# Performance work log

Measured on AMD Instinct MI355X. Metric: run time of the kernel, lower is better.

## Reference

```python
import jax, jax.numpy as jnp
import numpy as np

N_NODES = 50000


def _gcn_conv(x, src, dst, norm, W, b):
    # x: [N, F_in], src/dst: [E+N] (self loops included), norm: [E+N]
    h = x @ W                                   # [N, F_out]
    msg = h[src] * norm[:, None]                # [E+N, F_out] gather + scale
    out = jax.ops.segment_sum(msg, dst, num_segments=N_NODES)  # scatter-add
    return out + b


def _norm_coeffs(edge_index, n_nodes):
    # PyG GCNConv: add self loops, deg over dst (col), norm = d^-1/2[src]*d^-1/2[dst]
    loops = jnp.arange(n_nodes, dtype=edge_index.dtype)
    src = jnp.concatenate([edge_index[0], loops])
    dst = jnp.concatenate([edge_index[1], loops])
    deg = jax.ops.segment_sum(jnp.ones_like(dst, dtype=jnp.float32), dst,
                              num_segments=n_nodes)
    dinv = jnp.where(deg > 0, jax.lax.rsqrt(jnp.maximum(deg, 1.0)), 0.0)
    norm = dinv[src] * dinv[dst]
    return src, dst, norm


def setup_inputs() -> dict:
    key = jax.random.key(0)
    ks = jax.random.split(key, 8)
    F_in, F_hid, E = 128, 128, 600000
    x = jax.random.normal(ks[0], (N_NODES, F_in), dtype=jnp.float32)
    edge_index = jax.random.randint(ks[1], (2, E), 0, N_NODES, dtype=jnp.int32)
    s1 = 1.0 / np.sqrt(F_in)
    s2 = 1.0 / np.sqrt(F_hid)
    W1 = jax.random.uniform(ks[2], (F_in, F_hid), jnp.float32, -s1, s1)
    b1 = jnp.zeros((F_hid,), jnp.float32)
    W2 = jax.random.uniform(ks[3], (F_hid, F_hid), jnp.float32, -s2, s2)
    b2 = jnp.zeros((F_hid,), jnp.float32)
    W3 = jax.random.uniform(ks[4], (F_hid, F_hid), jnp.float32, -s2, s2)
    b3 = jnp.zeros((F_hid,), jnp.float32)
    return {"x": x, "edge_index": edge_index,
            "W1": W1, "b1": b1, "W2": W2, "b2": b2, "W3": W3, "b3": b3}


def reference(x, edge_index, W1, b1, W2, b2, W3, b3):
    src, dst, norm = _norm_coeffs(edge_index, N_NODES)
    h = jax.nn.relu(_gcn_conv(x, src, dst, norm, W1, b1))
    h = jax.nn.relu(_gcn_conv(h, src, dst, norm, W2, b2))
    h = _gcn_conv(h, src, dst, norm, W3, b3)
    # original forward returns (x, h) with x rebound to h (identical arrays)
    return (h, h)
```

## Files before the change

### kernel.cpp

```cpp
#include <hip/hip_runtime.h>

#define NNODES 50000
#define FDIM 128
#define KELL 40

typedef float f4 __attribute__((ext_vector_type(4)));
typedef float f2 __attribute__((ext_vector_type(2)));
typedef short short8 __attribute__((ext_vector_type(8)));
typedef uint uint4v __attribute__((ext_vector_type(4)));
typedef uint uint2v __attribute__((ext_vector_type(2)));

__global__ __launch_bounds__(256) void k_fill(const int* __restrict__ src,
                                              const int* __restrict__ dst,
                                              int* __restrict__ fill,
                                              int* __restrict__ col, int E) {
    int i = blockIdx.x * 256 + threadIdx.x;
    int e0 = i * 2;
    if (e0 + 1 < E) {
        int2 s2 = *(const int2*)(src + e0);
        int2 d2 = *(const int2*)(dst + e0);
        int slot0 = atomicAdd(&fill[d2.x], 1);
        int slot1 = atomicAdd(&fill[d2.y], 1);
        if (slot0 < KELL) col[d2.x * KELL + slot0] = s2.x;
        if (slot1 < KELL) col[d2.y * KELL + slot1] = s2.y;
    } else if (e0 < E) {
        int d = dst[e0];
        int slot = atomicAdd(&fill[d], 1);
        if (slot < KELL) col[d * KELL + slot] = src[e0];
    }
}

__device__ __forceinline__ void split2(float x0, float x1, unsigned& hi, unsigned& lo) {
    unsigned u0 = __float_as_uint(x0), u1 = __float_as_uint(x1);
    unsigned h0 = u0 & 0xffff0000u, h1 = u1 & 0xffff0000u;
    hi = h1 | (h0 >> 16);
    float l0 = x0 - __uint_as_float(h0);
    float l1 = x1 - __uint_as_float(h1);
    lo = (__float_as_uint(l1) & 0xffff0000u) | (__float_as_uint(l0) >> 16);
}

__device__ __forceinline__ unsigned pack2(float lo, float hi) {
    unsigned ul = __float_as_uint(lo);
    unsigned uh = __float_as_uint(hi);
    ul += 0x7fffu + ((ul >> 16) & 1u);
    uh += 0x7fffu + ((uh >> 16) & 1u);
    return (ul >> 16) | (uh & 0xffff0000u);
}

__device__ __forceinline__ f4 dec(uint2v v) {
    f4 r;
    r.x = __uint_as_float(v.x << 16);
    r.y = __uint_as_float(v.x & 0xffff0000u);
    r.z = __uint_as_float(v.y << 16);
    r.w = __uint_as_float(v.y & 0xffff0000u);
    return r;
}

__global__ __launch_bounds__(256) void k_prepw(const float* __restrict__ W1,
                                               const float* __restrict__ W2,
                                               const float* __restrict__ W3,
                                               unsigned* __restrict__ wpk) {
    int y = blockIdx.y;
    const float* W = (y == 0) ? W1 : (y == 1) ? W2 : W3;
    unsigned* dh = wpk + (size_t)y * 16384;
    unsigned* dl = dh + 8192;
    int p = blockIdx.x * 256 + threadIdx.x;
    int jp = p & 3;
    int l = (p >> 2) & 63;
    int st = p >> 8;
    int s = st >> 3, t = st & 7;
    int k0 = ((l >> 4) << 3) + (jp << 1) + (s << 5);
    int n = (t << 4) + (l & 15);
    float x0 = W[k0 * 128 + n];
    float x1 = W[(k0 + 1) * 128 + n];
    unsigned hi, lo;
    split2(x0, x1, hi, lo);
    dh[p] = hi;
    dl[p] = lo;
}

__global__ __launch_bounds__(256, 4) void k_gemm(const float* __restrict__ A,
                                                 const unsigned* __restrict__ wsrc,
                                                 unsigned* __restrict__ H, int nrows) {
    int tid = threadIdx.x;
    int w = tid >> 6, l = tid & 63;
    int m16 = l & 15, q = l >> 4;
    int rbase = blockIdx.x * 64 + w * 16;
    int row = rbase + m16;
    int rowc = row > nrows - 1 ? nrows - 1 : row;

    union u8 { unsigned u[4]; uint4v uv; short8 v; };
    u8 ah[4], al[4];
    const f4* A4 = (const f4*)A;
#pragma unroll
    for (int s = 0; s < 4; ++s) {
        f4 a0 = A4[(size_t)rowc * 32 + s * 8 + q * 2];
        f4 a1 = A4[(size_t)rowc * 32 + s * 8 + q * 2 + 1];
        split2(a0.x, a0.y, ah[s].u[0], al[s].u[0]);
        split2(a0.z, a0.w, ah[s].u[1], al[s].u[1]);
        split2(a1.x, a1.y, ah[s].u[2], al[s].u[2]);
        split2(a1.z, a1.w, ah[s].u[3], al[s].u[3]);
    }

    f4 acc[8];
#pragma unroll
    for (int t = 0; t < 8; ++t) acc[t] = (f4)0.0f;

    const uint4v* wg4 = (const uint4v*)wsrc;
#pragma unroll
    for (int s = 0; s < 4; ++s) {
#pragma unroll
        for (int t = 0; t < 8; ++t) {
            u8 bh, bl;
            bh.uv = wg4[(s * 8 + t) * 64 + l];
            bl.uv = wg4[2048 + (s * 8 + t) * 64 + l];
            acc[t] = __builtin_amdgcn_mfma_f32_16x16x32_bf16(ah[s].v, bh.v, acc[t], 0, 0, 0);
            acc[t] = __builtin_amdgcn_mfma_f32_16x16x32_bf16(al[s].v, bh.v, acc[t], 0, 0, 0);
            acc[t] = __builtin_amdgcn_mfma_f32_16x16x32_bf16(ah[s].v, bl.v, acc[t], 0, 0, 0);
        }
    }

#pragma unroll
    for (int up = 0; up < 4; ++up) {
#pragma unroll
        for (int r = 0; r < 4; ++r) {
            int rr = rbase + q * 4 + r;
            if (rr < nrows)
                H[(size_t)rr * 64 + up * 16 + m16] =
                    pack2(acc[2 * up][r], acc[2 * up + 1][r]);
        }
    }
}

__global__ __launch_bounds__(256, 4) void k_agg_gemm(const unsigned* __restrict__ hin,
                                                     const int* __restrict__ fill,
                                                     const int* __restrict__ col,
                                                     const float* __restrict__ bias,
                                                     const unsigned* __restrict__ wsrc,
                                                     unsigned* __restrict__ hout) {
    __shared__ float As[64][132];
    int tid = threadIdx.x;
    int w = tid >> 6, l = tid & 63;
    int half = l >> 5;
    int sl = l & 31;
    int hb = half * 32;
    int nbase = blockIdx.x * 64 + w * 16;

    const uint2v* h2 = (const uint2v*)hin;
#pragma unroll 1
    for (int it = 0; it < 8; ++it) {
        int n = nbase + it * 2 + half;
        int nc = n >= NNODES ? NNODES - 1 : n;
        int deg = fill[nc];
        int c = deg < KELL ? deg : KELL;
        float di = rsqrtf(1.0f + (float)deg);
        f4 a = di * dec(h2[(size_t)nc * 32 + sl]);

        int beg = nc * KELL;
        int cv = 0;
        float wv = 0.0f;
        if (sl < c) {
            cv = col[beg + sl];
            wv = rsqrtf(1.0f + (float)fill[cv]);
        }
        int j = 0;
#pragma unroll 1
        for (; j + 8 <= c; j += 8) {
            int s0 = __shfl(cv, hb + j);
            int s1 = __shfl(cv, hb + j + 1);
            int s2 = __shfl(cv, hb + j + 2);
            int s3 = __shfl(cv, hb + j + 3);
            int s4 = __shfl(cv, hb + j + 4);
            int s5 = __shfl(cv, hb + j + 5);
            int s6 = __shfl(cv, hb + j + 6);
            int s7 = __shfl(cv, hb + j + 7);
            float w0 = __shfl(wv, hb + j);
            float w1 = __shfl(wv, hb + j + 1);
            float w2 = __shfl(wv, hb + j + 2);
            float w3 = __shfl(wv, hb + j + 3);
            float w4 = __shfl(wv, hb + j + 4);
            float w5 = __shfl(wv, hb + j + 5);
            float w6 = __shfl(wv, hb + j + 6);
            float w7 = __shfl(wv, hb + j + 7);
            uint2v v0 = h2[(size_t)s0 * 32 + sl];
            uint2v v1 = h2[(size_t)s1 * 32 + sl];
            uint2v v2 = h2[(size_t)s2 * 32 + sl];
            uint2v v3 = h2[(size_t)s3 * 32 + sl];
            uint2v v4 = h2[(size_t)s4 * 32 + sl];
            uint2v v5 = h2[(size_t)s5 * 32 + sl];
            uint2v v6 = h2[(size_t)s6 * 32 + sl];
            uint2v v7 = h2[(size_t)s7 * 32 + sl];
            a += w0 * dec(v0); a += w1 * dec(v1); a += w2 * dec(v2); a += w3 * dec(v3);
            a += w4 * dec(v4); a += w5 * dec(v5); a += w6 * dec(v6); a += w7 * dec(v7);
        }
#pragma unroll 1
        for (; j + 4 <= c; j += 4) {
            int s0 = __shfl(cv, hb + j);
            int s1 = __shfl(cv, hb + j + 1);
            int s2 = __shfl(cv, hb + j + 2);
            int s3 = __shfl(cv, hb + j + 3);
            float w0 = __shfl(wv, hb + j);
            float w1 = __shfl(wv, hb + j + 1);
            float w2 = __shfl(wv, hb + j + 2);
            float w3 = __shfl(wv, hb + j + 3);
            uint2v v0 = h2[(size_t)s0 * 32 + sl];
            uint2v v1 = h2[(size_t)s1 * 32 + sl];
            uint2v v2 = h2[(size_t)s2 * 32 + sl];
            uint2v v3 = h2[(size_t)s3 * 32 + sl];
            a += w0 * dec(v0); a += w1 * dec(v1); a += w2 * dec(v2); a += w3 * dec(v3);
        }
#pragma unroll 1
        for (; j < c; ++j) {
            int s = __shfl(cv, hb + j);
            float wgt = __shfl(wv, hb + j);
            a += wgt * dec(h2[(size_t)s * 32 + sl]);
        }

        int u = sl >> 3;
        int m = (sl & 7) * 2;
        int c0 = u * 32 + m;
        f2 b0 = *(const f2*)(bias + c0);
        f2 b1v = *(const f2*)(bias + c0 + 16);
        f2 o0, o1;
        o0.x = fmaxf(di * a.x + b0.x, 0.0f);
        o0.y = fmaxf(di * a.z + b0.y, 0.0f);
        o1.x = fmaxf(di * a.y + b1v.x, 0.0f);
        o1.y = fmaxf(di * a.w + b1v.y, 0.0f);
        int rl = w * 16 + it * 2 + half;
        *(f2*)&As[rl][c0] = o0;
        *(f2*)&As[rl][c0 + 16] = o1;
    }

    int m16 = l & 15, q = l >> 4;
    int rl = w * 16 + m16;
    union u8 { unsigned u[4]; uint4v uv; short8 v; };
    u8 ah[4], al[4];
#pragma unroll
    for (int s = 0; s < 4; ++s) {
        f4 a0 = *(const f4*)&As[rl][s * 32 + q * 8];
        f4 a1 = *(const f4*)&As[rl][s * 32 + q * 8 + 4];
        split2(a0.x, a0.y, ah[s].u[0], al[s].u[0]);
        split2(a0.z, a0.w, ah[s].u[1], al[s].u[1]);
        split2(a1.x, a1.y, ah[s].u[2], al[s].u[2]);
        split2(a1.z, a1.w, ah[s].u[3], al[s].u[3]);
    }

    f4 acc[8];
#pragma unroll
    for (int t = 0; t < 8; ++t) acc[t] = (f4)0.0f;

    const uint4v* wg4 = (const uint4v*)wsrc;
#pragma unroll
    for (int s = 0; s < 4; ++s) {
#pragma unroll
        for (int t = 0; t < 8; ++t) {
            u8 bh, bl;
            bh.uv = wg4[(s * 8 + t) * 64 + l];
            bl.uv = wg4[2048 + (s * 8 + t) * 64 + l];
            acc[t] = __builtin_amdgcn_mfma_f32_16x16x32_bf16(ah[s].v, bh.v, acc[t], 0, 0, 0);
            acc[t] = __builtin_amdgcn_mfma_f32_16x16x32_bf16(al[s].v, bh.v, acc[t], 0, 0, 0);
            acc[t] = __builtin_amdgcn_mfma_f32_16x16x32_bf16(ah[s].v, bl.v, acc[t], 0, 0, 0);
        }
    }

    int rbase = blockIdx.x * 64 + w * 16;
#pragma unroll
    for (int up = 0; up < 4; ++up) {
#pragma unroll
        for (int r = 0; r < 4; ++r) {
            int rr = rbase + q * 4 + r;
            if (rr < NNODES)
                hout[(size_t)rr * 64 + up * 16 + m16] =
                    pack2(acc[2 * up][r], acc[2 * up + 1][r]);
        }
    }
}

__global__ __launch_bounds__(256) void k_agg(const unsigned* __restrict__ hpk,
                                             const int* __restrict__ fill,
                                             const int* __restrict__ col,
                                             const float* __restrict__ bias,
                                             float* __restrict__ out,
                                             float* __restrict__ out2, int relu) {
    int gw = (blockIdx.x * 256 + threadIdx.x) >> 6;
    int lane = threadIdx.x & 63;
    int half = lane >> 5;
    int sl = lane & 31;
    int hb = half * 32;
    int n = gw * 2 + half;
    if (n >= NNODES) return;
    int deg = fill[n];
    int c = deg < KELL ? deg : KELL;
    float di = rsqrtf(1.0f + (float)deg);

    const uint2v* h2 = (const uint2v*)hpk;
    f4 a = di * dec(h2[(size_t)n * 32 + sl]);

    int beg = n * KELL;
    {
        int cv = 0;
        float wv = 0.0f;
        if (sl < c) {
            cv = col[beg + sl];
            wv = rsqrtf(1.0f + (float)fill[cv]);
        }
        int j = 0;
#pragma unroll 1
        for (; j + 8 <= c; j += 8) {
            int s0 = __shfl(cv, hb + j);
            int s1 = __shfl(cv, hb + j + 1);
            int s2 = __shfl(cv, hb + j + 2);
            int s3 = __shfl(cv, hb + j + 3);
            int s4 = __shfl(cv, hb + j + 4);
            int s5 = __shfl(cv, hb + j + 5);
            int s6 = __shfl(cv, hb + j + 6);
            int s7 = __shfl(cv, hb + j + 7);
            float w0 = __shfl(wv, hb + j);
            float w1 = __shfl(wv, hb + j + 1);
            float w2 = __shfl(wv, hb + j + 2);
            float w3 = __shfl(wv, hb + j + 3);
            float w4 = __shfl(wv, hb + j + 4);
            float w5 = __shfl(wv, hb + j + 5);
            float w6 = __shfl(wv, hb + j + 6);
            float w7 = __shfl(wv, hb + j + 7);
            uint2v v0 = h2[(size_t)s0 * 32 + sl];
            uint2v v1 = h2[(size_t)s1 * 32 + sl];
            uint2v v2 = h2[(size_t)s2 * 32 + sl];
            uint2v v3 = h2[(size_t)s3 * 32 + sl];
            uint2v v4 = h2[(size_t)s4 * 32 + sl];
            uint2v v5 = h2[(size_t)s5 * 32 + sl];
            uint2v v6 = h2[(size_t)s6 * 32 + sl];
            uint2v v7 = h2[(size_t)s7 * 32 + sl];
            a += w0 * dec(v0); a += w1 * dec(v1); a += w2 * dec(v2); a += w3 * dec(v3);
            a += w4 * dec(v4); a += w5 * dec(v5); a += w6 * dec(v6); a += w7 * dec(v7);
        }
#pragma unroll 1
        for (; j + 4 <= c; j += 4) {
            int s0 = __shfl(cv, hb + j);
            int s1 = __shfl(cv, hb + j + 1);
            int s2 = __shfl(cv, hb + j + 2);
            int s3 = __shfl(cv, hb + j + 3);
            float w0 = __shfl(wv, hb + j);
            float w1 = __shfl(wv, hb + j + 1);
            float w2 = __shfl(wv, hb + j + 2);
            float w3 = __shfl(wv, hb + j + 3);
            uint2v v0 = h2[(size_t)s0 * 32 + sl];
            uint2v v1 = h2[(size_t)s1 * 32 + sl];
            uint2v v2 = h2[(size_t)s2 * 32 + sl];
            uint2v v3 = h2[(size_t)s3 * 32 + sl];
            a += w0 * dec(v0); a += w1 * dec(v1); a += w2 * dec(v2); a += w3 * dec(v3);
        }
#pragma unroll 1
        for (; j < c; ++j) {
            int s = __shfl(cv, hb + j);
            float wgt = __shfl(wv, hb + j);
            a += wgt * dec(h2[(size_t)s * 32 + sl]);
        }
    }

    int u = sl >> 3;
    int m = (sl & 7) * 2;
    int c0 = u * 32 + m;
    f2 b0 = *(const f2*)(bias + c0);
    f2 b1 = *(const f2*)(bias + c0 + 16);
    f2 o0, o1;
    o0.x = di * a.x + b0.x;
    o0.y = di * a.z + b0.y;
    o1.x = di * a.y + b1.x;
    o1.y = di * a.w + b1.y;
    if (relu) {
        o0.x = fmaxf(o0.x, 0.0f);
        o0.y = fmaxf(o0.y, 0.0f);
        o1.x = fmaxf(o1.x, 0.0f);
        o1.y = fmaxf(o1.y, 0.0f);
    }
    float* orow = out + (size_t)n * FDIM;
    *(f2*)(orow + c0) = o0;
    *(f2*)(orow + c0 + 16) = o1;
    if (out2) {
        float* orow2 = out2 + (size_t)n * FDIM;
        *(f2*)(orow2 + c0) = o0;
        *(f2*)(orow2 + c0 + 16) = o1;
    }
}

extern "C" void kernel_launch(void* const* d_in, const int* in_sizes, int n_in,
                              void* d_out, int out_size, void* d_ws, size_t ws_size,
                              hipStream_t stream) {
    const float* x  = (const float*)d_in[0];
    const int*   ei = (const int*)d_in[1];
    const float* W1 = (const float*)d_in[2];
    const float* b1 = (const float*)d_in[3];
    const float* W2 = (const float*)d_in[4];
    const float* b2 = (const float*)d_in[5];
    const float* W3 = (const float*)d_in[6];
    const float* b3 = (const float*)d_in[7];
    int E = in_sizes[1] / 2;
    const int* srcp = ei;
    const int* dstp = ei + E;
    float* outf = (float*)d_out;

    unsigned* hpkA = (unsigned*)d_ws;
    int*      fill = (int*)(hpkA + (size_t)NNODES * 64);
    int*      col  = fill + NNODES;
    unsigned* wpk  = (unsigned*)(col + (size_t)NNODES * KELL);
    unsigned* hpkB = (unsigned*)outf;

    (void)hipMemsetAsync(fill, 0, sizeof(int) * NNODES, stream);

    int eb = (E / 2 + 255) / 256;
    int gb = (NNODES + 63) / 64;
    int ab = (NNODES / 2 * 64 + 255) / 256;

    k_prepw<<<dim3(32, 3), 256, 0, stream>>>(W1, W2, W3, wpk);
    k_fill<<<eb, 256, 0, stream>>>(srcp, dstp, fill, col, E);

    k_gemm<<<gb, 256, 0, stream>>>(x, wpk, hpkA, NNODES);
    k_agg_gemm<<<gb, 256, 0, stream>>>(hpkA, fill, col, b1, wpk + 16384, hpkB);
    k_agg_gemm<<<gb, 256, 0, stream>>>(hpkB, fill, col, b2, wpk + 32768, hpkA);
    k_agg<<<ab, 256, 0, stream>>>(hpkA, fill, col, b3, outf,
                                  outf + (size_t)NNODES * FDIM, 0);
}
```

Measured before the change: 249.3 us.

## Merge setup launches and retile fused aggregate-GEMM to 16-row blocks

Replaces the memset and weight-prep launch with one kernel that both converts weights and zeroes the fill counters. The first GEMM and the edge bucketing now run as disjoint block ranges of a single launch. The fused aggregate+GEMM kernel now uses 128-thread blocks covering 16 nodes, with the two waves splitting the output columns after a __syncthreads. This cuts launch overhead and gives finer-grained blocks for better load balance, at the cost of each block re-reading the weight tiles and adding a barrier.

```diff
diff --git a/kernel.cpp b/kernel.cpp
--- a/kernel.cpp
+++ b/kernel.cpp
@@ -10,11 +10,73 @@
 typedef uint uint4v __attribute__((ext_vector_type(4)));
 typedef uint uint2v __attribute__((ext_vector_type(2)));
 
-__global__ __launch_bounds__(256) void k_fill(const int* __restrict__ src,
-                                              const int* __restrict__ dst,
-                                              int* __restrict__ fill,
-                                              int* __restrict__ col, int E) {
-    int i = blockIdx.x * 256 + threadIdx.x;
+__device__ __forceinline__ void split2(float x0, float x1, unsigned& hi, unsigned& lo) {
+    unsigned u0 = __float_as_uint(x0), u1 = __float_as_uint(x1);
+    unsigned h0 = u0 & 0xffff0000u, h1 = u1 & 0xffff0000u;
+    hi = h1 | (h0 >> 16);
+    float l0 = x0 - __uint_as_float(h0);
+    float l1 = x1 - __uint_as_float(h1);
+    lo = (__float_as_uint(l1) & 0xffff0000u) | (__float_as_uint(l0) >> 16);
+}
+
+__device__ __forceinline__ unsigned pack2(float lo, float hi) {
+    unsigned ul = __float_as_uint(lo);
+    unsigned uh = __float_as_uint(hi);
+    ul += 0x7fffu + ((ul >> 16) & 1u);
+    uh += 0x7fffu + ((uh >> 16) & 1u);
+    return (ul >> 16) | (uh & 0xffff0000u);
+}
+
+__device__ __forceinline__ f4 dec(uint2v v) {
+    f4 r;
+    r.x = __uint_as_float(v.x << 16);
+    r.y = __uint_as_float(v.x & 0xffff0000u);
+    r.z = __uint_as_float(v.y << 16);
+    r.w = __uint_as_float(v.y & 0xffff0000u);
+    return r;
+}
+
+__device__ __forceinline__ void prepw_body(const float* __restrict__ W,
+                                           unsigned* __restrict__ dh, int p) {
+    unsigned* dl = dh + 8192;
+    int jp = p & 3;
+    int l = (p >> 2) & 63;
+    int st = p >> 8;
+    int s = st >> 3, t = st & 7;
+    int k0 = ((l >> 4) << 3) + (jp << 1) + (s << 5);
+    int n = (t << 4) + (l & 15);
+    float x0 = W[k0 * 128 + n];
+    float x1 = W[(k0 + 1) * 128 + n];
+    unsigned hi, lo;
+    split2(x0, x1, hi, lo);
+    dh[p] = hi;
+    dl[p] = lo;
+}
+
+#define NB_PREP 96
+#define NB_ZERO 196
+
+__global__ __launch_bounds__(256) void k_pre(const float* __restrict__ W1,
+                                             const float* __restrict__ W2,
+                                             const float* __restrict__ W3,
+                                             unsigned* __restrict__ wpk,
+                                             int* __restrict__ fill) {
+    int bid = blockIdx.x;
+    int tid = threadIdx.x;
+    if (bid < NB_PREP) {
+        int y = bid >> 5;
+        const float* W = (y == 0) ? W1 : (y == 1) ? W2 : W3;
+        prepw_body(W, wpk + (size_t)y * 16384, (bid & 31) * 256 + tid);
+    } else {
+        int i = (bid - NB_PREP) * 256 + tid;
+        if (i < NNODES) fill[i] = 0;
+    }
+}
+
+__device__ __forceinline__ void fill_body(const int* __restrict__ src,
+                                          const int* __restrict__ dst,
+                                          int* __restrict__ fill,
+                                          int* __restrict__ col, int E, int i) {
     int e0 = i * 2;
     if (e0 + 1 < E) {
         int2 s2 = *(const int2*)(src + e0);
@@ -30,62 +92,13 @@
     }
 }
 
-__device__ __forceinline__ void split2(float x0, float x1, unsigned& hi, unsigned& lo) {
-    unsigned u0 = __float_as_uint(x0), u1 = __float_as_uint(x1);
-    unsigned h0 = u0 & 0xffff0000u, h1 = u1 & 0xffff0000u;
-    hi = h1 | (h0 >> 16);
-    float l0 = x0 - __uint_as_float(h0);
-    float l1 = x1 - __uint_as_float(h1);
-    lo = (__float_as_uint(l1) & 0xffff0000u) | (__float_as_uint(l0) >> 16);
-}
-
-__device__ __forceinline__ unsigned pack2(float lo, float hi) {
-    unsigned ul = __float_as_uint(lo);
-    unsigned uh = __float_as_uint(hi);
-    ul += 0x7fffu + ((ul >> 16) & 1u);
-    uh += 0x7fffu + ((uh >> 16) & 1u);
-    return (ul >> 16) | (uh & 0xffff0000u);
-}
-
-__device__ __forceinline__ f4 dec(uint2v v) {
-    f4 r;
-    r.x = __uint_as_float(v.x << 16);
-    r.y = __uint_as_float(v.x & 0xffff0000u);
-    r.z = __uint_as_float(v.y << 16);
-    r.w = __uint_as_float(v.y & 0xffff0000u);
-    return r;
-}
-
-__global__ __launch_bounds__(256) void k_prepw(const float* __restrict__ W1,
-                                               const float* __restrict__ W2,
-                                               const float* __restrict__ W3,
-                                               unsigned* __restrict__ wpk) {
-    int y = blockIdx.y;
-    const float* W = (y == 0) ? W1 : (y == 1) ? W2 : W3;
-    unsigned* dh = wpk + (size_t)y * 16384;
-    unsigned* dl = dh + 8192;
-    int p = blockIdx.x * 256 + threadIdx.x;
-    int jp = p & 3;
-    int l = (p >> 2) & 63;
-    int st = p >> 8;
-    int s = st >> 3, t = st & 7;
-    int k0 = ((l >> 4) << 3) + (jp << 1) + (s << 5);
-    int n = (t << 4) + (l & 15);
-    float x0 = W[k0 * 128 + n];
-    float x1 = W[(k0 + 1) * 128 + n];
-    unsigned hi, lo;
-    split2(x0, x1, hi, lo);
-    dh[p] = hi;
-    dl[p] = lo;
-}
-
-__global__ __launch_bounds__(256, 4) void k_gemm(const float* __restrict__ A,
-                                                 const unsigned* __restrict__ wsrc,
-                                                 unsigned* __restrict__ H, int nrows) {
-    int tid = threadIdx.x;
+__device__ __forceinline__ void gemm1_body(const float* __restrict__ A,
+                                           const unsigned* __restrict__ wsrc,
+                                           unsigned* __restrict__ H, int nrows,
+                                           int bid, int tid) {
     int w = tid >> 6, l = tid & 63;
     int m16 = l & 15, q = l >> 4;
-    int rbase = blockIdx.x * 64 + w * 16;
+    int rbase = bid * 64 + w * 16;
     int row = rbase + m16;
     int rowc = row > nrows - 1 ? nrows - 1 : row;
 
@@ -132,31 +145,47 @@
     }
 }
 
-__global__ __launch_bounds__(256, 4) void k_agg_gemm(const unsigned* __restrict__ hin,
-                                                     const int* __restrict__ fill,
-                                                     const int* __restrict__ col,
-                                                     const float* __restrict__ bias,
-                                                     const unsigned* __restrict__ wsrc,
-                                                     unsigned* __restrict__ hout) {
-    __shared__ float As[64][132];
+__global__ __launch_bounds__(256, 4) void k_fillgemm(const float* __restrict__ x,
+                                                     const int* __restrict__ src,
+                                                     const int* __restrict__ dst,
+                                                     int* __restrict__ fill,
+                                                     int* __restrict__ col, int E, int gb,
+                                                     const unsigned* __restrict__ wpk,
+                                                     unsigned* __restrict__ H) {
+    int bid = blockIdx.x;
+    int tid = threadIdx.x;
+    if (bid < gb) {
+        gemm1_body(x, wpk, H, NNODES, bid, tid);
+    } else {
+        fill_body(src, dst, fill, col, E, (bid - gb) * 256 + tid);
+    }
+}
+
+__global__ __launch_bounds__(128, 5) void k_fused(const unsigned* __restrict__ hin,
+                                                  const int* __restrict__ fill,
+                                                  const int* __restrict__ col,
+                                                  const float* __restrict__ bias,
+                                                  const unsigned* __restrict__ wsrc,
+                                                  unsigned* __restrict__ hout) {
+    __shared__ float As[16][132];
     int tid = threadIdx.x;
     int w = tid >> 6, l = tid & 63;
     int half = l >> 5;
     int sl = l & 31;
     int hb = half * 32;
-    int nbase = blockIdx.x * 64 + w * 16;
+    int nbase = blockIdx.x * 16;
 
     const uint2v* h2 = (const uint2v*)hin;
 #pragma unroll 1
-    for (int it = 0; it < 8; ++it) {
-        int n = nbase + it * 2 + half;
-        int nc = n >= NNODES ? NNODES - 1 : n;
-        int deg = fill[nc];
+    for (int it = 0; it < 4; ++it) {
+        int rl = w * 8 + it * 2 + half;
+        int n = nbase + rl;
+        int deg = fill[n];
         int c = deg < KELL ? deg : KELL;
         float di = rsqrtf(1.0f + (float)deg);
-        f4 a = di * dec(h2[(size_t)nc * 32 + sl]);
-
-        int beg = nc * KELL;
+        f4 a = di * dec(h2[(size_t)n * 32 + sl]);
+
+        int beg = n * KELL;
         int cv = 0;
         float wv = 0.0f;
         if (sl < c) {
@@ -226,52 +255,50 @@
         o0.y = fmaxf(di * a.z + b0.y, 0.0f);
         o1.x = fmaxf(di * a.y + b1v.x, 0.0f);
         o1.y = fmaxf(di * a.w + b1v.y, 0.0f);
-        int rl = w * 16 + it * 2 + half;
         *(f2*)&As[rl][c0] = o0;
         *(f2*)&As[rl][c0 + 16] = o1;
     }
+    __syncthreads();
 
     int m16 = l & 15, q = l >> 4;
-    int rl = w * 16 + m16;
     union u8 { unsigned u[4]; uint4v uv; short8 v; };
     u8 ah[4], al[4];
 #pragma unroll
     for (int s = 0; s < 4; ++s) {
-        f4 a0 = *(const f4*)&As[rl][s * 32 + q * 8];
-        f4 a1 = *(const f4*)&As[rl][s * 32 + q * 8 + 4];
+        f4 a0 = *(const f4*)&As[m16][s * 32 + q * 8];
+        f4 a1 = *(const f4*)&As[m16][s * 32 + q * 8 + 4];
         split2(a0.x, a0.y, ah[s].u[0], al[s].u[0]);
         split2(a0.z, a0.w, ah[s].u[1], al[s].u[1]);
         split2(a1.x, a1.y, ah[s].u[2], al[s].u[2]);
         split2(a1.z, a1.w, ah[s].u[3], al[s].u[3]);
     }
 
-    f4 acc[8];
-#pragma unroll
-    for (int t = 0; t < 8; ++t) acc[t] = (f4)0.0f;
+    f4 acc[4];
+#pragma unroll
+    for (int tt = 0; tt < 4; ++tt) acc[tt] = (f4)0.0f;
 
     const uint4v* wg4 = (const uint4v*)wsrc;
 #pragma unroll
     for (int s = 0; s < 4; ++s) {
 #pragma unroll
-        for (int t = 0; t < 8; ++t) {
+        for (int tt = 0; tt < 4; ++tt) {
+            int t = w * 4 + tt;
             u8 bh, bl;
             bh.uv = wg4[(s * 8 + t) * 64 + l];
             bl.uv = wg4[2048 + (s * 8 + t) * 64 + l];
-            acc[t] = __builtin_amdgcn_mfma_f32_16x16x32_bf16(ah[s].v, bh.v, acc[t], 0, 0, 0);
-            acc[t] = __builtin_amdgcn_mfma_f32_16x16x32_bf16(al[s].v, bh.v, acc[t], 0, 0, 0);
-            acc[t] = __builtin_amdgcn_mfma_f32_16x16x32_bf16(ah[s].v, bl.v, acc[t], 0, 0, 0);
-        }
-    }
-
-    int rbase = blockIdx.x * 64 + w * 16;
-#pragma unroll
-    for (int up = 0; up < 4; ++up) {
+            acc[tt] = __builtin_amdgcn_mfma_f32_16x16x32_bf16(ah[s].v, bh.v, acc[tt], 0, 0, 0);
+            acc[tt] = __builtin_amdgcn_mfma_f32_16x16x32_bf16(al[s].v, bh.v, acc[tt], 0, 0, 0);
+            acc[tt] = __builtin_amdgcn_mfma_f32_16x16x32_bf16(ah[s].v, bl.v, acc[tt], 0, 0, 0);
+        }
+    }
+
+#pragma unroll
+    for (int p = 0; p < 2; ++p) {
 #pragma unroll
         for (int r = 0; r < 4; ++r) {
-            int rr = rbase + q * 4 + r;
-            if (rr < NNODES)
-                hout[(size_t)rr * 64 + up * 16 + m16] =
-                    pack2(acc[2 * up][r], acc[2 * up + 1][r]);
+            int rr = nbase + q * 4 + r;
+            hout[(size_t)rr * 64 + (2 * w + p) * 16 + m16] =
+                pack2(acc[2 * p][r], acc[2 * p + 1][r]);
         }
     }
 }
@@ -281,7 +308,7 @@
                                              const int* __restrict__ col,
                                              const float* __restrict__ bias,
                                              float* __restrict__ out,
-                                             float* __restrict__ out2, int relu) {
+                                             float* __restrict__ out2) {
     int gw = (blockIdx.x * 256 + threadIdx.x) >> 6;
     int lane = threadIdx.x & 63;
     int half = lane >> 5;
@@ -368,20 +395,12 @@
     o0.y = di * a.z + b0.y;
     o1.x = di * a.y + b1.x;
     o1.y = di * a.w + b1.y;
-    if (relu) {
-        o0.x = fmaxf(o0.x, 0.0f);
-        o0.y = fmaxf(o0.y, 0.0f);
-        o1.x = fmaxf(o1.x, 0.0f);
-        o1.y = fmaxf(o1.y, 0.0f);
-    }
     float* orow = out + (size_t)n * FDIM;
     *(f2*)(orow + c0) = o0;
     *(f2*)(orow + c0 + 16) = o1;
-    if (out2) {
-        float* orow2 = out2 + (size_t)n * FDIM;
-        *(f2*)(orow2 + c0) = o0;
-        *(f2*)(orow2 + c0 + 16) = o1;
-    }
+    float* orow2 = out2 + (size_t)n * FDIM;
+    *(f2*)(orow2 + c0) = o0;
+    *(f2*)(orow2 + c0 + 16) = o1;
 }
 
 extern "C" void kernel_launch(void* const* d_in, const int* in_sizes, int n_in,
@@ -406,18 +425,16 @@
     unsigned* wpk  = (unsigned*)(col + (size_t)NNODES * KELL);
     unsigned* hpkB = (unsigned*)outf;
 
-    (void)hipMemsetAsync(fill, 0, sizeof(int) * NNODES, stream);
-
     int eb = (E / 2 + 255) / 256;
     int gb = (NNODES + 63) / 64;
+    int fb = NNODES / 16;
     int ab = (NNODES / 2 * 64 + 255) / 256;
 
-    k_prepw<<<dim3(32, 3), 256, 0, stream>>>(W1, W2, W3, wpk);
-    k_fill<<<eb, 256, 0, stream>>>(srcp, dstp, fill, col, E);
-
-    k_gemm<<<gb, 256, 0, stream>>>(x, wpk, hpkA, NNODES);
-    k_agg_gemm<<<gb, 256, 0, stream>>>(hpkA, fill, col, b1, wpk + 16384, hpkB);
-    k_agg_gemm<<<gb, 256, 0, stream>>>(hpkB, fill, col, b2, wpk + 32768, hpkA);
+    k_pre<<<NB_PREP + NB_ZERO, 256, 0, stream>>>(W1, W2, W3, wpk, fill);
+    k_fillgemm<<<gb + eb, 256, 0, stream>>>(x, srcp, dstp, fill, col, E, gb,
+                                            wpk, hpkA);
+    k_fused<<<fb, 128, 0, stream>>>(hpkA, fill, col, b1, wpk + 16384, hpkB);
+    k_fused<<<fb, 128, 0, stream>>>(hpkB, fill, col, b2, wpk + 32768, hpkA);
     k_agg<<<ab, 256, 0, stream>>>(hpkA, fill, col, b3, outf,
-                                  outf + (size_t)NNODES * FDIM, 0);
-}
+                                  outf + (size_t)NNODES * FDIM);
+}
```

New measurement: 220.6 us. 11.5% less time.
